# Kernel tuning notes

Measured on AMD Instinct MI355X. Metric: run time of the kernel, lower is better.

## Reference

```python
import jax, jax.numpy as jnp
from jax import lax
import numpy as np

B, T, E, D, U = 64, 2048, 512, 1024, 128


def setup_inputs() -> dict:
    key = jax.random.key(0)
    ks = jax.random.split(key, 12)
    s = 0.05
    queries = jax.random.normal(ks[0], (B, 1, D), jnp.float32)
    prev = jax.random.uniform(ks[1], (B, T), jnp.float32)
    prev = prev / prev.sum(-1, keepdims=True)  # alignment-like (sums to 1)
    enc = jax.random.normal(ks[2], (B, T, E), jnp.float32)
    lengths = jax.random.randint(ks[3], (B,), 1, T + 1)
    conv_w = jax.random.normal(ks[4], (U, 1, 3), jnp.float32) * s   # (out,in,k)
    conv_b = jax.random.normal(ks[5], (U,), jnp.float32) * s
    Wq = jax.random.normal(ks[6], (U, D), jnp.float32) * s          # query_layer weight
    Wk = jax.random.normal(ks[7], (U, E), jnp.float32) * s          # key_layer weight
    v_w = jax.random.normal(ks[8], (1, U), jnp.float32) * s         # v weight
    v_b = jax.random.normal(ks[9], (1,), jnp.float32) * s           # v bias
    b = jax.random.uniform(ks[10], (U,), jnp.float32)               # nn.Parameter(torch.rand)
    return dict(queries=queries, previous_alignments=prev, encoder_output=enc,
                conv_w=conv_w, conv_b=conv_b, Wq=Wq, Wk=Wk, v_w=v_w, v_b=v_b,
                b=b, lengths=lengths)


def reference(queries, previous_alignments, encoder_output, conv_w, conv_b,
              Wq, Wk, v_w, v_b, b, lengths):
    Bt, Tt, Et = encoder_output.shape
    # set_memory: proj_key and mask
    proj_key = jnp.einsum('bte,ue->btu', encoder_output, Wk)          # (B,T,U)
    mask = jnp.arange(Tt)[None, :] >= lengths[:, None]                # (B,T)
    # conv1d on previous alignments, kernel 3, padding 1
    conv = lax.conv_general_dilated(previous_alignments[:, None, :], conv_w,
                                    window_strides=(1,), padding=[(1, 1)],
                                    dimension_numbers=('NCH', 'OIH', 'NCH'))
    conv_attn = (conv + conv_b[None, :, None]).transpose(0, 2, 1)     # (B,T,U)
    q_proj = jnp.einsum('bqd,ud->bqu', queries, Wq)                   # (B,1,U)
    w = jnp.tanh(q_proj + proj_key + conv_attn + b)                   # (B,T,U)
    score = jnp.einsum('btu,u->bt', w, v_w[0]) + v_b[0]               # (B,T)
    score = jnp.where(mask, -jnp.inf, score)
    attn_weight = jax.nn.softmax(score, axis=-1)                      # (B,T)
    context = jnp.einsum('bt,bte->be', attn_weight, encoder_output)[:, None, :]  # (B,1,E)
    return context, attn_weight
```

## Files before the change

kernel.cpp:

```cpp
#include <hip/hip_runtime.h>
#include <hip/hip_bf16.h>

typedef __bf16 bf16x8 __attribute__((ext_vector_type(8)));
typedef float  f32x4  __attribute__((ext_vector_type(4)));

#define Bsz 64
#define Tdim 2048
#define Edim 512
#define Ddim 1024
#define Udim 128
#define CHUNK 256
#define NCHUNK 8

__device__ inline bf16x8 cvt8(float4 a, float4 b) {
    bf16x8 h;
    h[0] = (__bf16)a.x; h[1] = (__bf16)a.y; h[2] = (__bf16)a.z; h[3] = (__bf16)a.w;
    h[4] = (__bf16)b.x; h[5] = (__bf16)b.y; h[6] = (__bf16)b.z; h[7] = (__bf16)b.w;
    return h;
}

__device__ inline float fast_tanh(float x) {
    float e = __expf(2.f * x);
    return 1.f - __fdividef(2.f, e + 1.f);
}

__global__ __launch_bounds__(256) void k_prep(const float* __restrict__ q,
                                              const float* __restrict__ Wq,
                                              const float* __restrict__ bparam,
                                              const float* __restrict__ convb,
                                              const float* __restrict__ Wk,
                                              unsigned short* __restrict__ wkbf,
                                              float* __restrict__ qb) {
    int bid = blockIdx.x, tid = threadIdx.x;
    if (bid >= 256) {
        int cb = bid - 256;
        #pragma unroll
        for (int k = 0; k < 2; ++k) {
            int E = (cb * 256 + tid) * 2 + k;
            int c8 = E & 7;
            int u  = (E >> 3) & 127;
            int es = E >> 10;
            const float* src = Wk + (size_t)u * Edim + es * 64 + c8 * 8;
            float4 a = *reinterpret_cast<const float4*>(src);
            float4 b = *reinterpret_cast<const float4*>(src + 4);
            int dst = es * 16384 + ((u * 128 + c8 * 16) ^ ((u & 7) << 4));
            *reinterpret_cast<bf16x8*>(reinterpret_cast<char*>(wkbf) + dst) = cvt8(a, b);
        }
        return;
    }
    int wg   = bid * 4 + (tid >> 6);
    int lane = tid & 63;
    int b  = wg >> 4;
    int u0 = (wg & 15) * 8;
    const float* qr = q + (size_t)b * Ddim + lane * 16;
    float4 qv[4];
    #pragma unroll
    for (int i = 0; i < 4; ++i) qv[i] = *reinterpret_cast<const float4*>(qr + i * 4);
    float s[8];
    #pragma unroll
    for (int jj = 0; jj < 8; ++jj) {
        const float* wr = Wq + (size_t)(u0 + jj) * Ddim + lane * 16;
        float acc = 0.f;
        #pragma unroll
        for (int i = 0; i < 4; ++i) {
            float4 w = *reinterpret_cast<const float4*>(wr + i * 4);
            acc += qv[i].x * w.x + qv[i].y * w.y + qv[i].z * w.z + qv[i].w * w.w;
        }
        s[jj] = acc;
    }
    #pragma unroll
    for (int m = 32; m; m >>= 1) {
        #pragma unroll
        for (int jj = 0; jj < 8; ++jj) s[jj] += __shfl_xor(s[jj], m);
    }
    if (lane == 0) {
        #pragma unroll
        for (int jj = 0; jj < 8; ++jj)
            qb[b * 128 + u0 + jj] = s[jj] + bparam[u0 + jj] + convb[u0 + jj];
    }
}

__global__ __launch_bounds__(512, 4) void k_score_ctx(const float* __restrict__ enc,
                                                      const float* __restrict__ prev,
                                                      const unsigned short* __restrict__ wkbf,
                                                      const float* __restrict__ qb,
                                                      const float* __restrict__ conv_w,
                                                      const float* __restrict__ v_w,
                                                      const float* __restrict__ v_b,
                                                      const int* __restrict__ lengths,
                                                      float* __restrict__ score_out,
                                                      float* __restrict__ m_ws,
                                                      float* __restrict__ l_ws,
                                                      float* __restrict__ c_ws) {
    __shared__ alignas(16) unsigned short At[256 * 64];
    __shared__ alignas(16) unsigned short Bt[128 * 64];
    __shared__ float s_prev[258];
    __shared__ float s_qb[128];
    __shared__ float s_vw[128];
    __shared__ float s_cw[3][128];
    __shared__ float s_score[256];
    __shared__ float s_p[256];
    __shared__ float s_redm[4], s_redl[4];
    __shared__ alignas(16) float s_cred[3][128][4];

    const int tid   = threadIdx.x;
    const int b     = blockIdx.x;
    const int chunk = blockIdx.y;
    const int t0    = chunk * CHUNK;
    const int lane  = tid & 63, wid = tid >> 6;
    const int len   = lengths[b];
    const int pidx  = b * NCHUNK + chunk;

    if (t0 >= len) {
        if (tid == 0) { m_ws[pidx] = -3.4e38f; l_ws[pidx] = 0.f; }
        return;
    }

    if (tid < 128) {
        s_qb[tid]    = qb[b * 128 + tid];
        s_vw[tid]    = v_w[tid];
        s_cw[0][tid] = conv_w[tid * 3 + 0];
        s_cw[1][tid] = conv_w[tid * 3 + 1];
        s_cw[2][tid] = conv_w[tid * 3 + 2];
    }
    if (tid >= 128 && tid < 128 + 258) {
        int k = tid - 128;
        int idx = t0 - 1 + k;
        s_prev[k] = (idx >= 0 && idx < Tdim) ? prev[b * Tdim + idx] : 0.f;
    }

    const float* encb = enc + ((size_t)b * Tdim + t0) * Edim;

    f32x4 acc[2][8];
    #pragma unroll
    for (int m = 0; m < 2; ++m)
        #pragma unroll
        for (int n = 0; n < 8; ++n) acc[m][n] = (f32x4){0.f, 0.f, 0.f, 0.f};

    for (int es = 0; es < 8; ++es) {
        const int e0 = es * 64;
        {
            const char* wsrc = reinterpret_cast<const char*>(wkbf) + es * 16384 + tid * 16;
            char* bdst = reinterpret_cast<char*>(Bt) + tid * 16;
            __builtin_amdgcn_global_load_lds(
                (const __attribute__((address_space(1))) unsigned int*)(wsrc),
                (__attribute__((address_space(3))) unsigned int*)(bdst), 16, 0, 0);
            __builtin_amdgcn_global_load_lds(
                (const __attribute__((address_space(1))) unsigned int*)(wsrc + 8192),
                (__attribute__((address_space(3))) unsigned int*)(bdst + 8192), 16, 0, 0);
        }
        #pragma unroll
        for (int pass = 0; pass < 2; ++pass) {
            float4 ra[4];
            int lin0 = tid + pass * 1024;
            #pragma unroll
            for (int sl = 0; sl < 2; ++sl) {
                int lin = lin0 + sl * 512;
                int r = lin >> 3, c8 = lin & 7;
                const float* src = encb + (size_t)r * Edim + e0 + c8 * 8;
                ra[2 * sl]     = *reinterpret_cast<const float4*>(src);
                ra[2 * sl + 1] = *reinterpret_cast<const float4*>(src + 4);
            }
            #pragma unroll
            for (int sl = 0; sl < 2; ++sl) {
                int lin = lin0 + sl * 512;
                int r = lin >> 3, c8 = lin & 7;
                int off = (r * 128 + c8 * 16) ^ ((r & 7) << 4);
                *reinterpret_cast<bf16x8*>(reinterpret_cast<char*>(At) + off) =
                    cvt8(ra[2 * sl], ra[2 * sl + 1]);
            }
        }
        __syncthreads();
        #pragma unroll
        for (int kk = 0; kk < 2; ++kk) {
            bf16x8 af[2];
            #pragma unroll
            for (int m = 0; m < 2; ++m) {
                int ar = wid * 32 + m * 16 + (lane & 15);
                int abyte = (ar * 128 + kk * 64 + (lane >> 4) * 16) ^ ((ar & 7) << 4);
                af[m] = *reinterpret_cast<const bf16x8*>(reinterpret_cast<const char*>(At) + abyte);
            }
            #pragma unroll
            for (int n = 0; n < 8; ++n) {
                int br = n * 16 + (lane & 15);
                int bbyte = (br * 128 + kk * 64 + (lane >> 4) * 16) ^ ((br & 7) << 4);
                bf16x8 bv = *reinterpret_cast<const bf16x8*>(reinterpret_cast<const char*>(Bt) + bbyte);
                acc[0][n] = __builtin_amdgcn_mfma_f32_16x16x32_bf16(af[0], bv, acc[0][n], 0, 0, 0);
                acc[1][n] = __builtin_amdgcn_mfma_f32_16x16x32_bf16(af[1], bv, acc[1][n], 0, 0, 0);
            }
        }
        __syncthreads();
    }

    float sc[2][4] = {{0.f,0.f,0.f,0.f},{0.f,0.f,0.f,0.f}};
    #pragma unroll
    for (int m = 0; m < 2; ++m) {
        #pragma unroll
        for (int n = 0; n < 8; ++n) {
            int u = n * 16 + (lane & 15);
            float c0 = s_cw[0][u], c1 = s_cw[1][u], c2 = s_cw[2][u];
            float qbu = s_qb[u], vwu = s_vw[u];
            #pragma unroll
            for (int j = 0; j < 4; ++j) {
                int r = wid * 32 + m * 16 + (lane >> 4) * 4 + j;
                float conv = s_prev[r] * c0 + s_prev[r + 1] * c1 + s_prev[r + 2] * c2;
                sc[m][j] += vwu * fast_tanh(acc[m][n][j] + qbu + conv);
            }
        }
    }
    #pragma unroll
    for (int m = 0; m < 2; ++m)
        #pragma unroll
        for (int j = 0; j < 4; ++j) {
            sc[m][j] += __shfl_xor(sc[m][j], 1);
            sc[m][j] += __shfl_xor(sc[m][j], 2);
            sc[m][j] += __shfl_xor(sc[m][j], 4);
            sc[m][j] += __shfl_xor(sc[m][j], 8);
        }
    if ((lane & 15) == 0) {
        float vb = v_b[0];
        #pragma unroll
        for (int m = 0; m < 2; ++m) {
            int r = wid * 32 + m * 16 + (lane >> 4) * 4;
            #pragma unroll
            for (int j = 0; j < 4; ++j) {
                float s = sc[m][j] + vb;
                s_score[r + j] = s;
                score_out[b * Tdim + t0 + r + j] = s;
            }
        }
    }
    __syncthreads();

    float sv = 0.f;
    if (tid < 256) sv = (t0 + tid < len) ? s_score[tid] : -3.4e38f;
    {
        float m = (tid < 256) ? sv : -3.4e38f;
        #pragma unroll
        for (int s = 32; s; s >>= 1) m = fmaxf(m, __shfl_xor(m, s));
        if (tid < 256 && lane == 0) s_redm[wid] = m;
    }
    __syncthreads();
    float M = fmaxf(fmaxf(s_redm[0], s_redm[1]), fmaxf(s_redm[2], s_redm[3]));
    float p = 0.f;
    if (tid < 256) {
        p = (t0 + tid < len) ? __expf(sv - M) : 0.f;
        s_p[tid] = p;
    }
    {
        float l = (tid < 256) ? p : 0.f;
        #pragma unroll
        for (int s = 32; s; s >>= 1) l += __shfl_xor(l, s);
        if (tid < 256 && lane == 0) s_redl[wid] = l;
    }
    __syncthreads();
    if (tid == 0) {
        m_ws[pidx] = M;
        l_ws[pidx] = s_redl[0] + s_redl[1] + s_redl[2] + s_redl[3];
    }

    {
        int e4 = (tid & 127) * 4;
        int tg = tid >> 7;
        float4 a = make_float4(0.f, 0.f, 0.f, 0.f);
        #pragma unroll 4
        for (int t = tg; t < CHUNK; t += 4) {
            float pt = s_p[t];
            float4 v = *reinterpret_cast<const float4*>(encb + (size_t)t * Edim + e4);
            a.x += pt * v.x; a.y += pt * v.y; a.z += pt * v.z; a.w += pt * v.w;
        }
        if (tg > 0) *reinterpret_cast<float4*>(&s_cred[tg - 1][tid & 127][0]) = a;
        __syncthreads();
        if (tg == 0) {
            #pragma unroll
            for (int g = 0; g < 3; ++g) {
                float4 o = *reinterpret_cast<const float4*>(&s_cred[g][tid][0]);
                a.x += o.x; a.y += o.y; a.z += o.z; a.w += o.w;
            }
            *reinterpret_cast<float4*>(c_ws + (size_t)pidx * Edim + e4) = a;
        }
    }
}

__global__ __launch_bounds__(256) void k_combine(const float* __restrict__ m_ws,
                                                 const float* __restrict__ l_ws,
                                                 const float* __restrict__ c_ws,
                                                 const int* __restrict__ lengths,
                                                 float* __restrict__ ctx,
                                                 float* __restrict__ attn) {
    int b = blockIdx.x, tid = threadIdx.x;
    int lane = tid & 63, wid = tid >> 6;
    __shared__ float s_w[NCHUNK];
    __shared__ float sM, sinvL;

    if (wid == 0) {
        float mj = (lane < NCHUNK) ? m_ws[b * NCHUNK + lane] : -3.4e38f;
        float lj = (lane < NCHUNK) ? l_ws[b * NCHUNK + lane] : 0.f;
        float M = mj;
        #pragma unroll
        for (int s = 32; s; s >>= 1) M = fmaxf(M, __shfl_xor(M, s));
        float w = (lj > 0.f) ? __expf(mj - M) : 0.f;
        float L = lj * w;
        #pragma unroll
        for (int s = 32; s; s >>= 1) L += __shfl_xor(L, s);
        if (lane < NCHUNK) s_w[lane] = w;
        if (lane == 0) { sM = M; sinvL = 1.f / L; }
    }
    __syncthreads();
    float M = sM, invL = sinvL;

    {
        int e2 = tid * 2;
        float ax = 0.f, ay = 0.f;
        #pragma unroll
        for (int j = 0; j < NCHUNK; ++j) {
            float w = s_w[j];
            if (w != 0.f) {
                float2 v = *reinterpret_cast<const float2*>(c_ws + ((size_t)(b * NCHUNK + j)) * Edim + e2);
                ax += w * v.x; ay += w * v.y;
            }
        }
        *reinterpret_cast<float2*>(ctx + (size_t)b * Edim + e2) = make_float2(ax * invL, ay * invL);
    }

    int len = lengths[b];
    #pragma unroll
    for (int i = 0; i < Tdim / 256; ++i) {
        int t = tid + i * 256;
        float s = attn[(size_t)b * Tdim + t];
        attn[(size_t)b * Tdim + t] = (t < len) ? __expf(s - M) * invL : 0.f;
    }
}

extern "C" void kernel_launch(void* const* d_in, const int* in_sizes, int n_in,
                              void* d_out, int out_size, void* d_ws, size_t ws_size,
                              hipStream_t stream) {
    const float* queries = (const float*)d_in[0];
    const float* prev    = (const float*)d_in[1];
    const float* enc     = (const float*)d_in[2];
    const float* conv_w  = (const float*)d_in[3];
    const float* conv_b  = (const float*)d_in[4];
    const float* Wq      = (const float*)d_in[5];
    const float* Wk      = (const float*)d_in[6];
    const float* v_w     = (const float*)d_in[7];
    const float* v_b     = (const float*)d_in[8];
    const float* bparam  = (const float*)d_in[9];
    const int*   lengths = (const int*)d_in[10];

    float* out  = (float*)d_out;
    float* ctx  = out;
    float* attn = out + Bsz * Edim;

    char* ws = (char*)d_ws;
    unsigned short* wkbf = (unsigned short*)ws;
    float* qb   = (float*)(ws + 131072);
    float* m_ws = (float*)(ws + 163840);
    float* l_ws = (float*)(ws + 172032);
    float* c_ws = (float*)(ws + 196608);

    k_prep<<<272, 256, 0, stream>>>(queries, Wq, bparam, conv_b, Wk, wkbf, qb);
    k_score_ctx<<<dim3(Bsz, NCHUNK), 512, 0, stream>>>(enc, prev, wkbf, qb, conv_w, v_w, v_b,
                                                       lengths, attn, m_ws, l_ws, c_ws);
    k_combine<<<Bsz, 256, 0, stream>>>(m_ws, l_ws, c_ws, lengths, ctx, attn);
}
```

Measured before the change: 77.46 us.

## Load MFMA operands directly from global memory, dropping LDS staging

The score kernel no longer stages the encoder tile and the Wk tile in LDS. Each lane now loads its A fragment straight from global fp32 and converts it to bf16 in registers. The prep kernel pre-packs Wk into fragment order so each lane reads B fragments with a single contiguous 16-byte load. This removes the LDS writes, the LDS reads and the per-K-step barriers, but every wave now re-reads Wk from L2/L1 and the global loads are strided by row. Launch bounds are relaxed to 3 blocks per SM so more registers are available for the fully unrolled loop.

```diff
diff --git a/kernel.cpp b/kernel.cpp
--- a/kernel.cpp
+++ b/kernel.cpp
@@ -37,14 +37,15 @@
         #pragma unroll
         for (int k = 0; k < 2; ++k) {
             int E = (cb * 256 + tid) * 2 + k;
-            int c8 = E & 7;
-            int u  = (E >> 3) & 127;
-            int es = E >> 10;
-            const float* src = Wk + (size_t)u * Edim + es * 64 + c8 * 8;
+            int l  = E & 63;
+            int n  = (E >> 6) & 7;
+            int ks = E >> 9;
+            int u  = n * 16 + (l & 15);
+            int e  = ks * 32 + (l >> 4) * 8;
+            const float* src = Wk + (size_t)u * Edim + e;
             float4 a = *reinterpret_cast<const float4*>(src);
             float4 b = *reinterpret_cast<const float4*>(src + 4);
-            int dst = es * 16384 + ((u * 128 + c8 * 16) ^ ((u & 7) << 4));
-            *reinterpret_cast<bf16x8*>(reinterpret_cast<char*>(wkbf) + dst) = cvt8(a, b);
+            *reinterpret_cast<bf16x8*>(wkbf + (size_t)E * 8) = cvt8(a, b);
         }
         return;
     }
@@ -80,7 +81,7 @@
     }
 }
 
-__global__ __launch_bounds__(512, 4) void k_score_ctx(const float* __restrict__ enc,
+__global__ __launch_bounds__(512, 3) void k_score_ctx(const float* __restrict__ enc,
                                                       const float* __restrict__ prev,
                                                       const unsigned short* __restrict__ wkbf,
                                                       const float* __restrict__ qb,
@@ -92,8 +93,6 @@
                                                       float* __restrict__ m_ws,
                                                       float* __restrict__ l_ws,
                                                       float* __restrict__ c_ws) {
-    __shared__ alignas(16) unsigned short At[256 * 64];
-    __shared__ alignas(16) unsigned short Bt[128 * 64];
     __shared__ float s_prev[258];
     __shared__ float s_qb[128];
     __shared__ float s_vw[128];
@@ -131,66 +130,36 @@
 
     const float* encb = enc + ((size_t)b * Tdim + t0) * Edim;
 
+    const float* rowp[2];
+    #pragma unroll
+    for (int m = 0; m < 2; ++m)
+        rowp[m] = encb + (size_t)(wid * 32 + m * 16 + (lane & 15)) * Edim + (lane >> 4) * 8;
+    const unsigned short* wb = wkbf + lane * 8;
+
     f32x4 acc[2][8];
     #pragma unroll
     for (int m = 0; m < 2; ++m)
         #pragma unroll
         for (int n = 0; n < 8; ++n) acc[m][n] = (f32x4){0.f, 0.f, 0.f, 0.f};
 
-    for (int es = 0; es < 8; ++es) {
-        const int e0 = es * 64;
-        {
-            const char* wsrc = reinterpret_cast<const char*>(wkbf) + es * 16384 + tid * 16;
-            char* bdst = reinterpret_cast<char*>(Bt) + tid * 16;
-            __builtin_amdgcn_global_load_lds(
-                (const __attribute__((address_space(1))) unsigned int*)(wsrc),
-                (__attribute__((address_space(3))) unsigned int*)(bdst), 16, 0, 0);
-            __builtin_amdgcn_global_load_lds(
-                (const __attribute__((address_space(1))) unsigned int*)(wsrc + 8192),
-                (__attribute__((address_space(3))) unsigned int*)(bdst + 8192), 16, 0, 0);
-        }
-        #pragma unroll
-        for (int pass = 0; pass < 2; ++pass) {
-            float4 ra[4];
-            int lin0 = tid + pass * 1024;
-            #pragma unroll
-            for (int sl = 0; sl < 2; ++sl) {
-                int lin = lin0 + sl * 512;
-                int r = lin >> 3, c8 = lin & 7;
-                const float* src = encb + (size_t)r * Edim + e0 + c8 * 8;
-                ra[2 * sl]     = *reinterpret_cast<const float4*>(src);
-                ra[2 * sl + 1] = *reinterpret_cast<const float4*>(src + 4);
-            }
-            #pragma unroll
-            for (int sl = 0; sl < 2; ++sl) {
-                int lin = lin0 + sl * 512;
-                int r = lin >> 3, c8 = lin & 7;
-                int off = (r * 128 + c8 * 16) ^ ((r & 7) << 4);
-                *reinterpret_cast<bf16x8*>(reinterpret_cast<char*>(At) + off) =
-                    cvt8(ra[2 * sl], ra[2 * sl + 1]);
-            }
-        }
-        __syncthreads();
-        #pragma unroll
-        for (int kk = 0; kk < 2; ++kk) {
-            bf16x8 af[2];
-            #pragma unroll
-            for (int m = 0; m < 2; ++m) {
-                int ar = wid * 32 + m * 16 + (lane & 15);
-                int abyte = (ar * 128 + kk * 64 + (lane >> 4) * 16) ^ ((ar & 7) << 4);
-                af[m] = *reinterpret_cast<const bf16x8*>(reinterpret_cast<const char*>(At) + abyte);
-            }
-            #pragma unroll
-            for (int n = 0; n < 8; ++n) {
-                int br = n * 16 + (lane & 15);
-                int bbyte = (br * 128 + kk * 64 + (lane >> 4) * 16) ^ ((br & 7) << 4);
-                bf16x8 bv = *reinterpret_cast<const bf16x8*>(reinterpret_cast<const char*>(Bt) + bbyte);
-                acc[0][n] = __builtin_amdgcn_mfma_f32_16x16x32_bf16(af[0], bv, acc[0][n], 0, 0, 0);
-                acc[1][n] = __builtin_amdgcn_mfma_f32_16x16x32_bf16(af[1], bv, acc[1][n], 0, 0, 0);
-            }
-        }
-        __syncthreads();
-    }
+    #pragma unroll
+    for (int ks = 0; ks < 16; ++ks) {
+        bf16x8 af[2];
+        #pragma unroll
+        for (int m = 0; m < 2; ++m) {
+            float4 a0 = *reinterpret_cast<const float4*>(rowp[m] + ks * 32);
+            float4 a1 = *reinterpret_cast<const float4*>(rowp[m] + ks * 32 + 4);
+            af[m] = cvt8(a0, a1);
+        }
+        #pragma unroll
+        for (int n = 0; n < 8; ++n) {
+            bf16x8 bv = *reinterpret_cast<const bf16x8*>(wb + (size_t)(ks * 8 + n) * 512);
+            acc[0][n] = __builtin_amdgcn_mfma_f32_16x16x32_bf16(af[0], bv, acc[0][n], 0, 0, 0);
+            acc[1][n] = __builtin_amdgcn_mfma_f32_16x16x32_bf16(af[1], bv, acc[1][n], 0, 0, 0);
+        }
+    }
+
+    __syncthreads();
 
     float sc[2][4] = {{0.f,0.f,0.f,0.f},{0.f,0.f,0.f,0.f}};
     #pragma unroll
```

Measured after the change: 106.1 us. 1.37x slower.
